# Kernel optimization log

Measured on AMD Instinct MI355X. Metric: run time of the kernel, lower is better.

The kernel has to match this reference:

```python
import jax, jax.numpy as jnp
import numpy as np
import math

NHEAD = 8
OUT = 64
EF = 64
IN = 256
NTYPES = 5
NH = 50000
NT = 100000
E = 800000
NEG_SLOPE = 0.2

def _uniform(key, shape, fan):
    # matches reset(): uniform(-stdv, stdv), stdv = sqrt(6/(fan_in+fan_out)) over last two dims
    stdv = math.sqrt(6.0 / (shape[-2] + shape[-1]))
    return jax.random.uniform(key, shape, jnp.float32, -stdv, stdv)

def setup_inputs() -> dict:
    key = jax.random.key(0)
    ks = jax.random.split(key, 12)
    head_feature = jax.random.normal(ks[0], (NH, IN), jnp.float32)
    tail_feature = jax.random.normal(ks[1], (NT, IN), jnp.float32)
    head_ind = jax.random.randint(ks[2], (E,), 0, NH)
    tail_ind = jax.random.randint(ks[3], (E,), 0, NT)
    tmp_edge = jax.random.randint(ks[4], (E,), 0, NTYPES)
    edge_emb = _uniform(ks[5], (NTYPES, EF), None)
    W = _uniform(ks[6], (IN, OUT * NHEAD), None)
    W_e = _uniform(ks[7], (EF, EF * NHEAD), None)
    a_l = _uniform(ks[8], (1, NHEAD, OUT), None)
    a_r = _uniform(ks[9], (1, NHEAD, OUT), None)
    a_e = _uniform(ks[10], (1, NHEAD, EF), None)
    return {"head_feature": head_feature, "tail_feature": tail_feature,
            "head_ind": head_ind, "tail_ind": tail_ind, "tmp_edge": tmp_edge,
            "edge_emb": edge_emb, "W": W, "W_e": W_e,
            "a_l": a_l, "a_r": a_r, "a_e": a_e}

def reference(head_feature, tail_feature, head_ind, tail_ind, tmp_edge,
              edge_emb, W, W_e, a_l, a_r, a_e):
    n_head_nodes = head_feature.shape[0]
    # projections (dropout is identity in eval)
    h_head = (head_feature @ W).reshape(-1, NHEAD, OUT)   # [NH, H, D]
    h_tail = (tail_feature @ W).reshape(-1, NHEAD, OUT)   # [NT, H, D]
    e = (edge_emb @ W_e).reshape(-1, NHEAD, EF)           # [T, H, EF]
    # per-edge attention logits, all heads at once: [E, H]
    h_l = jnp.sum(a_l * h_head, axis=-1)[head_ind]
    h_r = jnp.sum(a_r * h_tail, axis=-1)[tail_ind]
    h_e = jnp.sum(a_e * e, axis=-1)[tmp_edge]
    att = jax.nn.leaky_relu(h_l + h_r + h_e, NEG_SLOPE)
    # sparse (per-destination-row) softmax, vectorized over heads
    seg_max = jax.ops.segment_max(att, head_ind, num_segments=n_head_nodes)
    att = jnp.exp(att - seg_max[head_ind])
    denom = jax.ops.segment_sum(att, head_ind, num_segments=n_head_nodes)
    att = att / denom[head_ind]                           # [E, H]
    # weighted aggregation per head (small fixed loop over heads)
    outs = [jax.ops.segment_sum(att[:, n:n + 1] * h_tail[tail_ind, n, :],
                                head_ind, num_segments=n_head_nodes)
            for n in range(NHEAD)]
    out = jnp.stack(outs, axis=1).reshape(n_head_nodes, -1)  # [NH, H*D]
    return out, att
```

## Files before the change

### kernel.cpp

```cpp
#include <hip/hip_runtime.h>

#define NH 50000
#define NT 100000
#define NE 800000
#define MPAD 100096

typedef __attribute__((ext_vector_type(8))) short bf16x8;
typedef __attribute__((ext_vector_type(4))) float f32x4;
typedef __attribute__((ext_vector_type(8))) unsigned short u16x8;

__device__ __forceinline__ unsigned short f2bf(float f){
  unsigned int u = __float_as_uint(f);
  u += 0x7FFFu + ((u >> 16) & 1u);
  return (unsigned short)(u >> 16);
}

__device__ __forceinline__ void fma8(float* acc, float w, uint4 pk){
  acc[0] += w*__uint_as_float(pk.x<<16); acc[1] += w*__uint_as_float(pk.x&0xFFFF0000u);
  acc[2] += w*__uint_as_float(pk.y<<16); acc[3] += w*__uint_as_float(pk.y&0xFFFF0000u);
  acc[4] += w*__uint_as_float(pk.z<<16); acc[5] += w*__uint_as_float(pk.z&0xFFFF0000u);
  acc[6] += w*__uint_as_float(pk.w<<16); acc[7] += w*__uint_as_float(pk.w&0xFFFF0000u);
}

__device__ __forceinline__ void gl2lds16(const unsigned short* g, unsigned short* l){
  __builtin_amdgcn_global_load_lds(
      (const __attribute__((address_space(1))) void*)g,
      (__attribute__((address_space(3))) void*)l, 16, 0, 0);
}

__global__ void k_prep(const float* __restrict__ W, const float* __restrict__ W_e,
                       const float* __restrict__ edge_emb,
                       const float* __restrict__ a_l, const float* __restrict__ a_r,
                       const float* __restrict__ a_e,
                       unsigned short* __restrict__ wlr_t,
                       float* __restrict__ h_e){
  __shared__ float s_al[512], s_ar[512], s_ae[512], s_wef[512];
  int t = threadIdx.x;
  for (int i=t;i<512;i+=256){ s_al[i]=a_l[i]; s_ar[i]=a_r[i]; s_ae[i]=a_e[i]; }
  __syncthreads();
  { int k = t;
    for (int h=0;h<8;h++){
      float accl=0.f, accr=0.f;
      for (int d=0; d<64; d++){
        float w = W[k*512 + h*64 + d];
        accl += w*s_al[h*64+d];
        accr += w*s_ar[h*64+d];
      }
      wlr_t[h*256 + k]     = f2bf(accl);
      wlr_t[(8+h)*256 + k] = f2bf(accr);
    }
  }
  if (t<64){
    for (int h=0;h<8;h++){
      float acc=0.f;
      for (int f=0; f<64; f++) acc += W_e[t*512 + h*64 + f]*s_ae[h*64+f];
      s_wef[t*8+h]=acc;
    }
  }
  __syncthreads();
  if (t<40){
    int ty=t>>3, h=t&7;
    float acc=0.f;
    for (int k2=0;k2<64;k2++) acc += edge_emb[ty*64+k2]*s_wef[k2*8+h];
    h_e[t]=acc;
  }
}

__global__ void k_wt(const float* __restrict__ W, unsigned short* __restrict__ Wt){
  int n = blockIdx.x, k = threadIdx.x;
  Wt[n*256+k] = f2bf(W[k*512+n]);
}

__global__ __launch_bounds__(256) void k_cvt(const float* __restrict__ A,
                                             unsigned short* __restrict__ Ab){
  size_t g = (size_t)blockIdx.x*256 + threadIdx.x;
  const float* src = A + g*8;
  float4 v0 = *(const float4*)(src);
  float4 v1 = *(const float4*)(src + 4);
  u16x8 s;
  s[0]=f2bf(v0.x); s[1]=f2bf(v0.y); s[2]=f2bf(v0.z); s[3]=f2bf(v0.w);
  s[4]=f2bf(v1.x); s[5]=f2bf(v1.y); s[6]=f2bf(v1.z); s[7]=f2bf(v1.w);
  *(u16x8*)(Ab + g*8) = s;
}

__global__ __launch_bounds__(256) void k_hl(const float* __restrict__ head_f,
      const unsigned short* __restrict__ wlr_t, float* __restrict__ h_l){
  __shared__ unsigned short As[256*64];
  __shared__ unsigned short Bs[16*256];
  int t = threadIdx.x;
  int wave = t>>6, lane = t&63;
  int lr = lane&15, lq = lane>>4;
  long r0 = (long)blockIdx.x*256;

#pragma unroll
  for (int i=0;i<2;i++){
    int q = i*256 + t;
    int c = q>>5, un = q&31;
    float4 v = *(const float4*)(wlr_t + c*256 + un*8);
    int u = un ^ (c&7);
    *(float4*)((char*)Bs + c*512 + u*16) = v;
  }

  f32x4 acc[4];
#pragma unroll
  for (int mf=0;mf<4;mf++) acc[mf]=(f32x4){0.f,0.f,0.f,0.f};

  for (int kt=0; kt<4; kt++){
    __syncthreads();
#pragma unroll
    for (int i=0;i<16;i++){
      int q = i*256+t;
      int row = q>>4, cg = q&15;
      long gr = r0 + row;
      float4 v = make_float4(0.f,0.f,0.f,0.f);
      if (gr < NH) v = *(const float4*)(head_f + gr*256 + kt*64 + cg*4);
      int u = (cg>>1) ^ (row&7);
      ushort4 sv;
      sv.x=f2bf(v.x); sv.y=f2bf(v.y); sv.z=f2bf(v.z); sv.w=f2bf(v.w);
      *(ushort4*)((char*)As + row*128 + u*16 + (cg&1)*8) = sv;
    }
    __syncthreads();
#pragma unroll
    for (int ks=0;ks<2;ks++){
      int un = kt*8 + ks*4 + lq;
      int cu = un ^ (lr&7);
      bf16x8 bfr = *(const bf16x8*)((const char*)Bs + lr*512 + cu*16);
#pragma unroll
      for (int mf=0;mf<4;mf++){
        int r = wave*64 + mf*16 + lr;
        int u = (ks*4+lq) ^ (r&7);
        bf16x8 afr = *(const bf16x8*)((const char*)As + r*128 + u*16);
        acc[mf] = __builtin_amdgcn_mfma_f32_16x16x32_bf16(afr, bfr, acc[mf], 0,0,0);
      }
    }
  }
#pragma unroll
  for (int mf=0;mf<4;mf++)
#pragma unroll
    for (int j=0;j<4;j++){
      long grow = r0 + wave*64 + mf*16 + lq*4 + j;
      if (grow < NH && lr < 8) h_l[grow*8+lr] = acc[mf][j];
    }
}

__global__ __launch_bounds__(256) void k_gemm3(const unsigned short* __restrict__ A_bf,
      const unsigned short* __restrict__ Wt, const float* __restrict__ a_r_g,
      unsigned short* __restrict__ Cout, float* __restrict__ h_r){
  __shared__ unsigned short As[2][128*64];
  int t = threadIdx.x;
  int wave = t>>6, lane = t&63;
  int lr = lane & 15, lq = lane >> 4;

  int bid = blockIdx.x;
  int wg  = (bid & 7)*391 + (bid >> 3);
  int m0 = (wg >> 2)*128;
  int n0 = (wg & 3)*128;
  int wm = (wave>>1)*64, wn = (wave&1)*64;

  f32x4 acc[4][4];
#pragma unroll
  for (int mf=0;mf<4;mf++)
#pragma unroll
    for (int nf=0;nf<4;nf++) acc[mf][nf] = (f32x4){0.f,0.f,0.f,0.f};

  bf16x8 bcur[8], bnxt[8];

#define STAGEA(buf, kt) do { \
    _Pragma("unroll") \
    for (int i=0;i<4;i++){ \
      int v = wave*256 + i*64 + lane; \
      int row = v>>3, un = (v&7) ^ (row&7); \
      gl2lds16(A_bf + (size_t)(m0+row)*256 + (kt)*64 + un*8, \
               &As[buf][(wave*256 + i*64)*8]); \
    } } while(0)

#define LOADB(kt, dst) do { \
    _Pragma("unroll") \
    for (int ks=0;ks<2;ks++) \
      _Pragma("unroll") \
      for (int nf=0;nf<4;nf++){ \
        int c = wn + nf*16 + lr; \
        (dst)[ks*4+nf] = *(const bf16x8*)(Wt + (size_t)(n0+c)*256 + ((kt)*8+ks*4+lq)*8); \
      } } while(0)

  STAGEA(0, 0);
  LOADB(0, bcur);
  __syncthreads();
  int cur = 0;
  for (int kt=0; kt<4; kt++){
    if (kt < 3){ STAGEA(cur^1, kt+1); LOADB(kt+1, bnxt); }
#pragma unroll
    for (int ks=0;ks<2;ks++){
      bf16x8 af[4];
#pragma unroll
      for (int mf=0;mf<4;mf++){
        int r = wm + mf*16 + lr;
        int u = (ks*4 + lq) ^ (r&7);
        af[mf] = *(const bf16x8*)((const char*)As[cur] + r*128 + u*16);
      }
#pragma unroll
      for (int mf=0;mf<4;mf++)
#pragma unroll
        for (int nf=0;nf<4;nf++)
          acc[mf][nf] = __builtin_amdgcn_mfma_f32_16x16x32_bf16(af[mf], bcur[ks*4+nf], acc[mf][nf], 0,0,0);
    }
    __syncthreads();
    if (kt < 3){
      cur ^= 1;
#pragma unroll
      for (int i=0;i<8;i++) bcur[i] = bnxt[i];
    }
  }
#undef STAGEA
#undef LOADB

  {
    int h = (n0 + wn) >> 6;
    float w[4];
#pragma unroll
    for (int nf=0;nf<4;nf++) w[nf] = a_r_g[h*64 + nf*16 + lr];
#pragma unroll
    for (int mf=0;mf<4;mf++)
#pragma unroll
      for (int j=0;j<4;j++){
        float s = acc[mf][0][j]*w[0] + acc[mf][1][j]*w[1]
                + acc[mf][2][j]*w[2] + acc[mf][3][j]*w[3];
        s += __shfl_xor(s, 1); s += __shfl_xor(s, 2);
        s += __shfl_xor(s, 4); s += __shfl_xor(s, 8);
        int gr = m0 + wm + mf*16 + lq*4 + j;
        if (lr == 0 && gr < NT) h_r[(size_t)gr*8 + h] = s;
      }
  }

  unsigned short* Cs = &As[0][0];
#pragma unroll
  for (int mf=0;mf<4;mf++)
#pragma unroll
    for (int nf=0;nf<4;nf++)
#pragma unroll
      for (int j=0;j<4;j++){
        int row = wm + mf*16 + lq*4 + j;
        int cb  = (wn + nf*16 + lr)*2;
        *(unsigned short*)((char*)Cs + row*256 + (cb ^ ((row&12)<<3))) = f2bf(acc[mf][nf][j]);
      }
  __syncthreads();
#pragma unroll
  for (int i=0;i<8;i++){
    int v = i*256 + t;
    int row = v>>4, u = v&15;
    uint4 val = *(const uint4*)((const char*)Cs + row*256 + ((u*16) ^ ((row&12)<<3)));
    *(uint4*)(Cout + (size_t)(m0+row)*512 + n0 + u*8) = val;
  }
}

__global__ void k_hist(const int* __restrict__ head_ind, int* __restrict__ cnt){
  int e = blockIdx.x*256 + threadIdx.x;
  atomicAdd(&cnt[head_ind[e]], 1);
}

__global__ void k_scan1(const int* __restrict__ cnt, int* __restrict__ bsum){
  __shared__ int s[256];
  int b=blockIdx.x, t=threadIdx.x, g=b*256+t;
  s[t] = (g<NH)? cnt[g] : 0;
  __syncthreads();
  for (int off=128; off>0; off>>=1){ if (t<off) s[t]+=s[t+off]; __syncthreads(); }
  if (t==0) bsum[b]=s[0];
}
__global__ void k_scan2(int* __restrict__ bsum, int nb){
  __shared__ int s[256];
  int t=threadIdx.x;
  int v = (t<nb)? bsum[t] : 0;
  s[t]=v; __syncthreads();
  for (int off=1; off<256; off<<=1){
    int u = (t>=off)? s[t-off] : 0; __syncthreads();
    s[t]+=u; __syncthreads();
  }
  if (t<nb) bsum[t] = s[t]-v;
}
__global__ void k_scan3(const int* __restrict__ cnt, const int* __restrict__ bsum,
                        int* __restrict__ offs, int* __restrict__ cur){
  __shared__ int s[256];
  int b=blockIdx.x, t=threadIdx.x, g=b*256+t;
  int v=(g<NH)? cnt[g] : 0;
  s[t]=v; __syncthreads();
  for (int off=1; off<256; off<<=1){
    int u=(t>=off)? s[t-off] : 0; __syncthreads();
    s[t]+=u; __syncthreads();
  }
  int excl = s[t]-v + bsum[b];
  if (g<NH){
    offs[g]=excl; cur[g]=excl;
    if (g==NH-1) offs[NH]=excl+v;
  }
}

__global__ void k_logit2(const int* __restrict__ head_ind, const int* __restrict__ tail_ind,
                         const int* __restrict__ tmp_edge,
                         const float* __restrict__ h_l, const float* __restrict__ h_r,
                         const float* __restrict__ h_e,
                         int* __restrict__ cur,
                         float* __restrict__ att_csr,
                         int* __restrict__ edge_of, int* __restrict__ tail_s){
  int g = blockIdx.x*256 + threadIdx.x;
  int e = g>>3, h = g&7, l = threadIdx.x&63;
  int hd = head_ind[e], tl = tail_ind[e], ty = tmp_edge[e];
  float v = h_l[hd*8+h] + h_r[(size_t)tl*8+h] + h_e[ty*8+h];
  v = v > 0.f ? v : 0.2f*v;
  int p = 0;
  if (h==0) p = atomicAdd(&cur[hd], 1);
  p = __shfl(p, l & ~7);
  att_csr[p*8+h] = v;
  if (h==0){ edge_of[p]=e; tail_s[p]=tl; }
}

__global__ __launch_bounds__(256) void k_agg3(const int* __restrict__ offs,
      const int* __restrict__ edge_of, const int* __restrict__ tail_s,
      const float* __restrict__ att_csr,
      const unsigned short* __restrict__ h_tail,
      float* __restrict__ att, float* __restrict__ out){
  int t = threadIdx.x;
  int l = t & 63;
  int i = blockIdx.x*4 + (t>>6);
  int h = l & 7, hq = l >> 3;
  int s0 = offs[i];
  int deg = offs[i+1] - s0;

  float m = -1e30f;
  for (int q = hq; q < deg; q += 8) m = fmaxf(m, att_csr[(s0+q)*8 + h]);
  m = fmaxf(m, __shfl_xor(m, 8));
  m = fmaxf(m, __shfl_xor(m, 16));
  m = fmaxf(m, __shfl_xor(m, 32));
  float sum = 0.f;
  for (int q = hq; q < deg; q += 8) sum += __expf(att_csr[(s0+q)*8 + h] - m);
  sum += __shfl_xor(sum, 8); sum += __shfl_xor(sum, 16); sum += __shfl_xor(sum, 32);
  float r = (deg > 0) ? 1.f/sum : 0.f;

  float mh = __shfl(m, hq), rh = __shfl(r, hq);
  bool wlane = (l & 7) == 0;
  float acc[8];
#pragma unroll
  for (int c=0;c<8;c++) acc[c]=0.f;

  int j = 0;
  for (; j+8 <= deg; j += 8){
    int   tt[8]; float aa[8]; uint4 rr[8];
#pragma unroll
    for (int q2=0;q2<8;q2++){ int p=s0+j+q2; tt[q2]=tail_s[p]; aa[q2]=att_csr[p*8+hq]; }
#pragma unroll
    for (int q2=0;q2<8;q2++) rr[q2] = *(const uint4*)(h_tail + (size_t)tt[q2]*512 + l*8);
#pragma unroll
    for (int q2=0;q2<8;q2++){
      float w = __expf(aa[q2]-mh)*rh;
      if (wlane) __builtin_nontemporal_store(w, &att[(size_t)edge_of[s0+j+q2]*8 + hq]);
      fma8(acc, w, rr[q2]);
    }
  }
  for (; j+2 <= deg; j += 2){
    int p0=s0+j, p1=p0+1;
    int t0=tail_s[p0], t1=tail_s[p1];
    float a0=att_csr[p0*8+hq], a1=att_csr[p1*8+hq];
    uint4 r0 = *(const uint4*)(h_tail + (size_t)t0*512 + l*8);
    uint4 r1 = *(const uint4*)(h_tail + (size_t)t1*512 + l*8);
    float w0=__expf(a0-mh)*rh, w1=__expf(a1-mh)*rh;
    if (wlane){
      __builtin_nontemporal_store(w0, &att[(size_t)edge_of[p0]*8 + hq]);
      __builtin_nontemporal_store(w1, &att[(size_t)edge_of[p1]*8 + hq]);
    }
    fma8(acc, w0, r0);
    fma8(acc, w1, r1);
  }
  if (j < deg){
    int p0 = s0+j;
    int t0 = tail_s[p0];
    float a0 = att_csr[p0*8 + hq];
    uint4 r0 = *(const uint4*)(h_tail + (size_t)t0*512 + l*8);
    float w0 = __expf(a0 - mh) * rh;
    if (wlane) __builtin_nontemporal_store(w0, &att[(size_t)edge_of[p0]*8 + hq]);
    fma8(acc, w0, r0);
  }
  float* o = out + (size_t)i*512 + l*8;
  f32x4 v0 = {acc[0],acc[1],acc[2],acc[3]};
  f32x4 v1 = {acc[4],acc[5],acc[6],acc[7]};
  __builtin_nontemporal_store(v0, (f32x4*)o);
  __builtin_nontemporal_store(v1, (f32x4*)(o+4));
}

extern "C" void kernel_launch(void* const* d_in, const int* in_sizes, int n_in,
                              void* d_out, int out_size, void* d_ws, size_t ws_size,
                              hipStream_t stream) {
  const float* head_f   = (const float*)d_in[0];
  const float* tail_f   = (const float*)d_in[1];
  const int*   head_ind = (const int*)d_in[2];
  const int*   tail_ind = (const int*)d_in[3];
  const int*   tmp_edge = (const int*)d_in[4];
  const float* edge_emb = (const float*)d_in[5];
  const float* W        = (const float*)d_in[6];
  const float* W_e      = (const float*)d_in[7];
  const float* a_l      = (const float*)d_in[8];
  const float* a_r      = (const float*)d_in[9];
  const float* a_e      = (const float*)d_in[10];

  float* out = (float*)d_out;
  float* att = out + (size_t)NH*512;
  unsigned short* A_bf = (unsigned short*)d_out;

  char* ws = (char*)d_ws;
  auto alloc = [&](size_t bytes)->char*{ char* p = ws; ws += (bytes+511)&~(size_t)511; return p; };
  unsigned short* Wt    = (unsigned short*)alloc((size_t)512*256*2);
  unsigned short* wlr_t = (unsigned short*)alloc((size_t)16*256*2);
  float* h_e            = (float*)alloc(512);
  float* h_l            = (float*)alloc((size_t)NH*8*4);
  float* h_r            = (float*)alloc((size_t)NT*8*4);
  unsigned short* h_tail= (unsigned short*)alloc((size_t)MPAD*512*2);
  int* cnt              = (int*)alloc((size_t)NH*4);
  int* offs             = (int*)alloc((size_t)(NH+1)*4);
  int* cur              = (int*)alloc((size_t)NH*4);
  int* bsum             = (int*)alloc(1024);
  int* edge_of          = (int*)alloc((size_t)NE*4);
  int* tail_s           = (int*)alloc((size_t)NE*4);
  float* att_csr        = (float*)alloc((size_t)NE*8*4);

  hipMemsetAsync(cnt, 0, (size_t)NH*4, stream);
  k_prep<<<1,256,0,stream>>>(W, W_e, edge_emb, a_l, a_r, a_e, wlr_t, h_e);
  k_wt<<<512,256,0,stream>>>(W, Wt);
  k_cvt<<<12500,256,0,stream>>>(tail_f, A_bf);
  k_hl<<<(NH+255)/256,256,0,stream>>>(head_f, wlr_t, h_l);
  k_gemm3<<<3128,256,0,stream>>>(A_bf, Wt, a_r, h_tail, h_r);
  k_hist<<<NE/256,256,0,stream>>>(head_ind, cnt);
  k_scan1<<<196,256,0,stream>>>(cnt, bsum);
  k_scan2<<<1,256,0,stream>>>(bsum, 196);
  k_scan3<<<196,256,0,stream>>>(cnt, bsum, offs, cur);
  k_logit2<<<NE*8/256,256,0,stream>>>(head_ind, tail_ind, tmp_edge, h_l, h_r, h_e,
                                      cur, att_csr, edge_of, tail_s);
  k_agg3<<<NH/4,256,0,stream>>>(offs, edge_of, tail_s, att_csr, h_tail, att, out);
}
```

Baseline: 438.5 us.

## Split aggregation into two half-head passes and stage full-K A tile in GEMM

The aggregation kernel is split into two launches, each gathering half of every h_tail row (heads 0-3, then 4-7), so each pass touches a smaller gathered working set that may stay in cache. The first pass also writes the normalized attention and saves per-row max and reciprocal sums for the second pass. The GEMM now loads the whole 128x256 A tile into LDS once instead of double-buffering K slices, with B fragments loaded per k-step and an occupancy hint. The split costs an extra launch, a second walk over the CSR index arrays, and more LDS per block.

```diff
diff --git a/kernel.cpp b/kernel.cpp
--- a/kernel.cpp
+++ b/kernel.cpp
@@ -8,6 +8,7 @@
 typedef __attribute__((ext_vector_type(8))) short bf16x8;
 typedef __attribute__((ext_vector_type(4))) float f32x4;
 typedef __attribute__((ext_vector_type(8))) unsigned short u16x8;
+typedef __attribute__((ext_vector_type(4))) unsigned int u32x4;
 
 __device__ __forceinline__ unsigned short f2bf(float f){
   unsigned int u = __float_as_uint(f);
@@ -15,11 +16,9 @@
   return (unsigned short)(u >> 16);
 }
 
-__device__ __forceinline__ void fma8(float* acc, float w, uint4 pk){
+__device__ __forceinline__ void fma4(float* acc, float w, uint2 pk){
   acc[0] += w*__uint_as_float(pk.x<<16); acc[1] += w*__uint_as_float(pk.x&0xFFFF0000u);
   acc[2] += w*__uint_as_float(pk.y<<16); acc[3] += w*__uint_as_float(pk.y&0xFFFF0000u);
-  acc[4] += w*__uint_as_float(pk.z<<16); acc[5] += w*__uint_as_float(pk.z&0xFFFF0000u);
-  acc[6] += w*__uint_as_float(pk.w<<16); acc[7] += w*__uint_as_float(pk.w&0xFFFF0000u);
 }
 
 __device__ __forceinline__ void gl2lds16(const unsigned short* g, unsigned short* l){
@@ -143,10 +142,10 @@
     }
 }
 
-__global__ __launch_bounds__(256) void k_gemm3(const unsigned short* __restrict__ A_bf,
+__global__ __launch_bounds__(256,2) void k_gemm4(const unsigned short* __restrict__ A_bf,
       const unsigned short* __restrict__ Wt, const float* __restrict__ a_r_g,
       unsigned short* __restrict__ Cout, float* __restrict__ h_r){
-  __shared__ unsigned short As[2][128*64];
+  __shared__ unsigned short As[128*256];
   int t = threadIdx.x;
   int wave = t>>6, lane = t&63;
   int lr = lane & 15, lq = lane >> 4;
@@ -157,62 +156,40 @@
   int n0 = (wg & 3)*128;
   int wm = (wave>>1)*64, wn = (wave&1)*64;
 
+#pragma unroll
+  for (int i=0;i<16;i++){
+    int v = i*256 + t;
+    int row = v>>5, un = (v&31) ^ (row&7);
+    gl2lds16(A_bf + (size_t)(m0+row)*256 + un*8, &As[(size_t)(i*256 + wave*64)*8]);
+  }
+
   f32x4 acc[4][4];
 #pragma unroll
   for (int mf=0;mf<4;mf++)
 #pragma unroll
     for (int nf=0;nf<4;nf++) acc[mf][nf] = (f32x4){0.f,0.f,0.f,0.f};
 
-  bf16x8 bcur[8], bnxt[8];
-
-#define STAGEA(buf, kt) do { \
-    _Pragma("unroll") \
-    for (int i=0;i<4;i++){ \
-      int v = wave*256 + i*64 + lane; \
-      int row = v>>3, un = (v&7) ^ (row&7); \
-      gl2lds16(A_bf + (size_t)(m0+row)*256 + (kt)*64 + un*8, \
-               &As[buf][(wave*256 + i*64)*8]); \
-    } } while(0)
-
-#define LOADB(kt, dst) do { \
-    _Pragma("unroll") \
-    for (int ks=0;ks<2;ks++) \
-      _Pragma("unroll") \
-      for (int nf=0;nf<4;nf++){ \
-        int c = wn + nf*16 + lr; \
-        (dst)[ks*4+nf] = *(const bf16x8*)(Wt + (size_t)(n0+c)*256 + ((kt)*8+ks*4+lq)*8); \
-      } } while(0)
-
-  STAGEA(0, 0);
-  LOADB(0, bcur);
-  __syncthreads();
-  int cur = 0;
-  for (int kt=0; kt<4; kt++){
-    if (kt < 3){ STAGEA(cur^1, kt+1); LOADB(kt+1, bnxt); }
-#pragma unroll
-    for (int ks=0;ks<2;ks++){
-      bf16x8 af[4];
-#pragma unroll
-      for (int mf=0;mf<4;mf++){
-        int r = wm + mf*16 + lr;
-        int u = (ks*4 + lq) ^ (r&7);
-        af[mf] = *(const bf16x8*)((const char*)As[cur] + r*128 + u*16);
-      }
-#pragma unroll
-      for (int mf=0;mf<4;mf++)
-#pragma unroll
-        for (int nf=0;nf<4;nf++)
-          acc[mf][nf] = __builtin_amdgcn_mfma_f32_16x16x32_bf16(af[mf], bcur[ks*4+nf], acc[mf][nf], 0,0,0);
-    }
-    __syncthreads();
-    if (kt < 3){
-      cur ^= 1;
-#pragma unroll
-      for (int i=0;i<8;i++) bcur[i] = bnxt[i];
-    }
-  }
-#undef STAGEA
-#undef LOADB
+  __syncthreads();
+
+#pragma unroll
+  for (int ks=0; ks<8; ks++){
+    bf16x8 bfr[4];
+#pragma unroll
+    for (int nf=0;nf<4;nf++)
+      bfr[nf] = *(const bf16x8*)(Wt + (size_t)(n0 + wn + nf*16 + lr)*256 + ks*32 + lq*8);
+    bf16x8 af[4];
+#pragma unroll
+    for (int mf=0;mf<4;mf++){
+      int r = wm + mf*16 + lr;
+      int un = (ks*4 + lq) ^ (r&7);
+      af[mf] = *(const bf16x8*)(As + (size_t)(r*32 + un)*8);
+    }
+#pragma unroll
+    for (int mf=0;mf<4;mf++)
+#pragma unroll
+      for (int nf=0;nf<4;nf++)
+        acc[mf][nf] = __builtin_amdgcn_mfma_f32_16x16x32_bf16(af[mf], bfr[nf], acc[mf][nf], 0,0,0);
+  }
 
   {
     int h = (n0 + wn) >> 6;
@@ -232,7 +209,8 @@
       }
   }
 
-  unsigned short* Cs = &As[0][0];
+  __syncthreads();
+  unsigned short* Cs = As;
 #pragma unroll
   for (int mf=0;mf<4;mf++)
 #pragma unroll
@@ -248,8 +226,8 @@
   for (int i=0;i<8;i++){
     int v = i*256 + t;
     int row = v>>4, u = v&15;
-    uint4 val = *(const uint4*)((const char*)Cs + row*256 + ((u*16) ^ ((row&12)<<3)));
-    *(uint4*)(Cout + (size_t)(m0+row)*512 + n0 + u*8) = val;
+    u32x4 val = *(const u32x4*)((const char*)Cs + row*256 + ((u*16) ^ ((row&12)<<3)));
+    *(u32x4*)(Cout + (size_t)(m0+row)*512 + n0 + u*8) = val;
   }
 }
 
@@ -313,76 +291,112 @@
   if (h==0){ edge_of[p]=e; tail_s[p]=tl; }
 }
 
-__global__ __launch_bounds__(256) void k_agg3(const int* __restrict__ offs,
+__global__ __launch_bounds__(256) void k_aggA(const int* __restrict__ offs,
       const int* __restrict__ edge_of, const int* __restrict__ tail_s,
       const float* __restrict__ att_csr,
       const unsigned short* __restrict__ h_tail,
+      float* __restrict__ mr,
       float* __restrict__ att, float* __restrict__ out){
   int t = threadIdx.x;
   int l = t & 63;
   int i = blockIdx.x*4 + (t>>6);
-  int h = l & 7, hq = l >> 3;
+  int h = l & 7, sq = l >> 3;
   int s0 = offs[i];
   int deg = offs[i+1] - s0;
 
   float m = -1e30f;
-  for (int q = hq; q < deg; q += 8) m = fmaxf(m, att_csr[(s0+q)*8 + h]);
+  for (int q = sq; q < deg; q += 8) m = fmaxf(m, att_csr[(s0+q)*8 + h]);
   m = fmaxf(m, __shfl_xor(m, 8));
   m = fmaxf(m, __shfl_xor(m, 16));
   m = fmaxf(m, __shfl_xor(m, 32));
   float sum = 0.f;
-  for (int q = hq; q < deg; q += 8) sum += __expf(att_csr[(s0+q)*8 + h] - m);
+  for (int q = sq; q < deg; q += 8) sum += __expf(att_csr[(s0+q)*8 + h] - m);
   sum += __shfl_xor(sum, 8); sum += __shfl_xor(sum, 16); sum += __shfl_xor(sum, 32);
   float r = (deg > 0) ? 1.f/sum : 0.f;
-
-  float mh = __shfl(m, hq), rh = __shfl(r, hq);
-  bool wlane = (l & 7) == 0;
-  float acc[8];
-#pragma unroll
-  for (int c=0;c<8;c++) acc[c]=0.f;
+  if (l < 8){ mr[(size_t)i*16 + l*2] = m; mr[(size_t)i*16 + l*2 + 1] = r; }
+
+  for (int q = sq; q < deg; q += 8){
+    int p = s0 + q;
+    float a = __expf(att_csr[p*8 + h] - m) * r;
+    __builtin_nontemporal_store(a, &att[(size_t)edge_of[p]*8 + h]);
+  }
+
+  int hw = l >> 4;
+  float mh = __shfl(m, hw), rh = __shfl(r, hw);
+  float acc[4];
+#pragma unroll
+  for (int c=0;c<4;c++) acc[c]=0.f;
 
   int j = 0;
-  for (; j+8 <= deg; j += 8){
-    int   tt[8]; float aa[8]; uint4 rr[8];
-#pragma unroll
-    for (int q2=0;q2<8;q2++){ int p=s0+j+q2; tt[q2]=tail_s[p]; aa[q2]=att_csr[p*8+hq]; }
-#pragma unroll
-    for (int q2=0;q2<8;q2++) rr[q2] = *(const uint4*)(h_tail + (size_t)tt[q2]*512 + l*8);
-#pragma unroll
-    for (int q2=0;q2<8;q2++){
-      float w = __expf(aa[q2]-mh)*rh;
-      if (wlane) __builtin_nontemporal_store(w, &att[(size_t)edge_of[s0+j+q2]*8 + hq]);
-      fma8(acc, w, rr[q2]);
-    }
-  }
-  for (; j+2 <= deg; j += 2){
-    int p0=s0+j, p1=p0+1;
-    int t0=tail_s[p0], t1=tail_s[p1];
-    float a0=att_csr[p0*8+hq], a1=att_csr[p1*8+hq];
-    uint4 r0 = *(const uint4*)(h_tail + (size_t)t0*512 + l*8);
-    uint4 r1 = *(const uint4*)(h_tail + (size_t)t1*512 + l*8);
-    float w0=__expf(a0-mh)*rh, w1=__expf(a1-mh)*rh;
-    if (wlane){
-      __builtin_nontemporal_store(w0, &att[(size_t)edge_of[p0]*8 + hq]);
-      __builtin_nontemporal_store(w1, &att[(size_t)edge_of[p1]*8 + hq]);
-    }
-    fma8(acc, w0, r0);
-    fma8(acc, w1, r1);
-  }
-  if (j < deg){
+  for (; j+4 <= deg; j += 4){
+    int p0=s0+j, p1=p0+1, p2=p0+2, p3=p0+3;
+    int t0=tail_s[p0], t1=tail_s[p1], t2=tail_s[p2], t3=tail_s[p3];
+    float a0=att_csr[p0*8+hw], a1=att_csr[p1*8+hw];
+    float a2=att_csr[p2*8+hw], a3=att_csr[p3*8+hw];
+    uint2 r0 = *(const uint2*)(h_tail + (size_t)t0*512 + l*4);
+    uint2 r1 = *(const uint2*)(h_tail + (size_t)t1*512 + l*4);
+    uint2 r2 = *(const uint2*)(h_tail + (size_t)t2*512 + l*4);
+    uint2 r3 = *(const uint2*)(h_tail + (size_t)t3*512 + l*4);
+    fma4(acc, __expf(a0-mh)*rh, r0);
+    fma4(acc, __expf(a1-mh)*rh, r1);
+    fma4(acc, __expf(a2-mh)*rh, r2);
+    fma4(acc, __expf(a3-mh)*rh, r3);
+  }
+  for (; j < deg; j++){
     int p0 = s0+j;
     int t0 = tail_s[p0];
-    float a0 = att_csr[p0*8 + hq];
-    uint4 r0 = *(const uint4*)(h_tail + (size_t)t0*512 + l*8);
-    float w0 = __expf(a0 - mh) * rh;
-    if (wlane) __builtin_nontemporal_store(w0, &att[(size_t)edge_of[p0]*8 + hq]);
-    fma8(acc, w0, r0);
-  }
-  float* o = out + (size_t)i*512 + l*8;
+    float a0 = att_csr[p0*8 + hw];
+    uint2 r0 = *(const uint2*)(h_tail + (size_t)t0*512 + l*4);
+    fma4(acc, __expf(a0 - mh)*rh, r0);
+  }
   f32x4 v0 = {acc[0],acc[1],acc[2],acc[3]};
-  f32x4 v1 = {acc[4],acc[5],acc[6],acc[7]};
-  __builtin_nontemporal_store(v0, (f32x4*)o);
-  __builtin_nontemporal_store(v1, (f32x4*)(o+4));
+  __builtin_nontemporal_store(v0, (f32x4*)(out + (size_t)i*512 + l*4));
+}
+
+__global__ __launch_bounds__(256) void k_aggB(const int* __restrict__ offs,
+      const int* __restrict__ tail_s,
+      const float* __restrict__ att_csr,
+      const unsigned short* __restrict__ h_tail,
+      const float* __restrict__ mr,
+      float* __restrict__ out){
+  int t = threadIdx.x;
+  int l = t & 63;
+  int i = blockIdx.x*4 + (t>>6);
+  int hw = 4 + (l >> 4);
+  int s0 = offs[i];
+  int deg = offs[i+1] - s0;
+
+  float2 st = *(const float2*)(mr + (size_t)i*16 + hw*2);
+  float mh = st.x, rh = st.y;
+
+  float acc[4];
+#pragma unroll
+  for (int c=0;c<4;c++) acc[c]=0.f;
+
+  int j = 0;
+  for (; j+4 <= deg; j += 4){
+    int p0=s0+j, p1=p0+1, p2=p0+2, p3=p0+3;
+    int t0=tail_s[p0], t1=tail_s[p1], t2=tail_s[p2], t3=tail_s[p3];
+    float a0=att_csr[p0*8+hw], a1=att_csr[p1*8+hw];
+    float a2=att_csr[p2*8+hw], a3=att_csr[p3*8+hw];
+    uint2 r0 = *(const uint2*)(h_tail + (size_t)t0*512 + 256 + l*4);
+    uint2 r1 = *(const uint2*)(h_tail + (size_t)t1*512 + 256 + l*4);
+    uint2 r2 = *(const uint2*)(h_tail + (size_t)t2*512 + 256 + l*4);
+    uint2 r3 = *(const uint2*)(h_tail + (size_t)t3*512 + 256 + l*4);
+    fma4(acc, __expf(a0-mh)*rh, r0);
+    fma4(acc, __expf(a1-mh)*rh, r1);
+    fma4(acc, __expf(a2-mh)*rh, r2);
+    fma4(acc, __expf(a3-mh)*rh, r3);
+  }
+  for (; j < deg; j++){
+    int p0 = s0+j;
+    int t0 = tail_s[p0];
+    float a0 = att_csr[p0*8 + hw];
+    uint2 r0 = *(const uint2*)(h_tail + (size_t)t0*512 + 256 + l*4);
+    fma4(acc, __expf(a0 - mh)*rh, r0);
+  }
+  f32x4 v0 = {acc[0],acc[1],acc[2],acc[3]};
+  __builtin_nontemporal_store(v0, (f32x4*)(out + (size_t)i*512 + 256 + l*4));
 }
 
 extern "C" void kernel_launch(void* const* d_in, const int* in_sizes, int n_in,
@@ -419,18 +433,20 @@
   int* edge_of          = (int*)alloc((size_t)NE*4);
   int* tail_s           = (int*)alloc((size_t)NE*4);
   float* att_csr        = (float*)alloc((size_t)NE*8*4);
+  float* mr             = (float*)alloc((size_t)NH*16*4);
 
   hipMemsetAsync(cnt, 0, (size_t)NH*4, stream);
   k_prep<<<1,256,0,stream>>>(W, W_e, edge_emb, a_l, a_r, a_e, wlr_t, h_e);
   k_wt<<<512,256,0,stream>>>(W, Wt);
   k_cvt<<<12500,256,0,stream>>>(tail_f, A_bf);
   k_hl<<<(NH+255)/256,256,0,stream>>>(head_f, wlr_t, h_l);
-  k_gemm3<<<3128,256,0,stream>>>(A_bf, Wt, a_r, h_tail, h_r);
+  k_gemm4<<<3128,256,0,stream>>>(A_bf, Wt, a_r, h_tail, h_r);
   k_hist<<<NE/256,256,0,stream>>>(head_ind, cnt);
   k_scan1<<<196,256,0,stream>>>(cnt, bsum);
   k_scan2<<<1,256,0,stream>>>(bsum, 196);
   k_scan3<<<196,256,0,stream>>>(cnt, bsum, offs, cur);
   k_logit2<<<NE*8/256,256,0,stream>>>(head_ind, tail_ind, tmp_edge, h_l, h_r, h_e,
                                       cur, att_csr, edge_of, tail_s);
-  k_agg3<<<NH/4,256,0,stream>>>(offs, edge_of, tail_s, att_csr, h_tail, att, out);
-}
+  k_aggA<<<NH/4,256,0,stream>>>(offs, edge_of, tail_s, att_csr, h_tail, mr, att, out);
+  k_aggB<<<NH/4,256,0,stream>>>(offs, tail_s, att_csr, h_tail, mr, out);
+}
```

Result: slower. 463.3 us (+5.7%).

## Merge prep/convert/histogram and GEMM/h_l kernels into block-dispatched launches; retune aggregation loop

Applied to the files above, without the earlier changes.

Independent small kernels (bf16 conversion, degree histogram, weight transpose, attention-vector prep) become one launch that picks its role by block index. The tail-projection GEMM and the h_l GEMM become a second combined launch sharing one LDS buffer. This cuts launch overhead and lets the independent stages overlap. The aggregation kernel now unrolls its gather by 4 instead of 8 and reads CSR streams with nontemporal loads. This adds a hazard: wlr_t is written by the prep block inside the same launch that converts data, and is then read in the next launch, so stream ordering still holds.

```diff
diff --git a/kernel.cpp b/kernel.cpp
--- a/kernel.cpp
+++ b/kernel.cpp
@@ -8,6 +8,7 @@
 typedef __attribute__((ext_vector_type(8))) short bf16x8;
 typedef __attribute__((ext_vector_type(4))) float f32x4;
 typedef __attribute__((ext_vector_type(8))) unsigned short u16x8;
+typedef __attribute__((ext_vector_type(4))) unsigned int u32x4;
 
 __device__ __forceinline__ unsigned short f2bf(float f){
   unsigned int u = __float_as_uint(f);
@@ -28,69 +29,180 @@
       (__attribute__((address_space(3))) void*)l, 16, 0, 0);
 }
 
-__global__ void k_prep(const float* __restrict__ W, const float* __restrict__ W_e,
-                       const float* __restrict__ edge_emb,
-                       const float* __restrict__ a_l, const float* __restrict__ a_r,
-                       const float* __restrict__ a_e,
-                       unsigned short* __restrict__ wlr_t,
-                       float* __restrict__ h_e){
+__global__ __launch_bounds__(256) void k_fuse1(
+      const float* __restrict__ tail_f, unsigned short* __restrict__ A_bf,
+      const int* __restrict__ head_ind, int* __restrict__ cnt,
+      const float* __restrict__ W, unsigned short* __restrict__ Wt,
+      const float* __restrict__ W_e, const float* __restrict__ edge_emb,
+      const float* __restrict__ a_l, const float* __restrict__ a_r,
+      const float* __restrict__ a_e,
+      unsigned short* __restrict__ wlr_t, float* __restrict__ h_e){
   __shared__ float s_al[512], s_ar[512], s_ae[512], s_wef[512];
+  int b = blockIdx.x, t = threadIdx.x;
+  if (b < 12500){
+    size_t g = (size_t)b*256 + t;
+    const float* src = tail_f + g*8;
+    float4 v0 = *(const float4*)(src);
+    float4 v1 = *(const float4*)(src + 4);
+    u16x8 s;
+    s[0]=f2bf(v0.x); s[1]=f2bf(v0.y); s[2]=f2bf(v0.z); s[3]=f2bf(v0.w);
+    s[4]=f2bf(v1.x); s[5]=f2bf(v1.y); s[6]=f2bf(v1.z); s[7]=f2bf(v1.w);
+    *(u16x8*)(A_bf + g*8) = s;
+  } else if (b < 15625){
+    int e = (b-12500)*256 + t;
+    atomicAdd(&cnt[head_ind[e]], 1);
+  } else if (b < 16137){
+    int n = b - 15625, k = t;
+    Wt[n*256+k] = f2bf(W[k*512+n]);
+  } else {
+    for (int i=t;i<512;i+=256){ s_al[i]=a_l[i]; s_ar[i]=a_r[i]; s_ae[i]=a_e[i]; }
+    __syncthreads();
+    { int k = t;
+      for (int h=0;h<8;h++){
+        float accl=0.f, accr=0.f;
+        for (int d=0; d<64; d++){
+          float w = W[k*512 + h*64 + d];
+          accl += w*s_al[h*64+d];
+          accr += w*s_ar[h*64+d];
+        }
+        wlr_t[h*256 + k]     = f2bf(accl);
+        wlr_t[(8+h)*256 + k] = f2bf(accr);
+      }
+    }
+    if (t<64){
+      for (int h=0;h<8;h++){
+        float acc=0.f;
+        for (int f=0; f<64; f++) acc += W_e[t*512 + h*64 + f]*s_ae[h*64+f];
+        s_wef[t*8+h]=acc;
+      }
+    }
+    __syncthreads();
+    if (t<40){
+      int ty=t>>3, h=t&7;
+      float acc=0.f;
+      for (int k2=0;k2<64;k2++) acc += edge_emb[ty*64+k2]*s_wef[k2*8+h];
+      h_e[t]=acc;
+    }
+  }
+}
+
+__device__ __forceinline__ void gemm3_body(unsigned short* smem, int bid,
+      const unsigned short* __restrict__ A_bf, const unsigned short* __restrict__ Wt,
+      const float* __restrict__ a_r_g, unsigned short* __restrict__ Cout,
+      float* __restrict__ h_r){
+  unsigned short* Asb[2] = { smem, smem + 8192 };
   int t = threadIdx.x;
-  for (int i=t;i<512;i+=256){ s_al[i]=a_l[i]; s_ar[i]=a_r[i]; s_ae[i]=a_e[i]; }
+  int wave = t>>6, lane = t&63;
+  int lr = lane & 15, lq = lane >> 4;
+
+  int wg  = (bid & 7)*391 + (bid >> 3);
+  int m0 = (wg >> 2)*128;
+  int n0 = (wg & 3)*128;
+  int wm = (wave>>1)*64, wn = (wave&1)*64;
+
+  f32x4 acc[4][4];
+#pragma unroll
+  for (int mf=0;mf<4;mf++)
+#pragma unroll
+    for (int nf=0;nf<4;nf++) acc[mf][nf] = (f32x4){0.f,0.f,0.f,0.f};
+
+  bf16x8 bcur[8], bnxt[8];
+
+#define STAGEA(buf, kt) do { \
+    _Pragma("unroll") \
+    for (int i=0;i<4;i++){ \
+      int v = wave*256 + i*64 + lane; \
+      int row = v>>3, un = (v&7) ^ (row&7); \
+      gl2lds16(A_bf + (size_t)(m0+row)*256 + (kt)*64 + un*8, \
+               &Asb[buf][(wave*256 + i*64)*8]); \
+    } } while(0)
+
+#define LOADB(kt, dst) do { \
+    _Pragma("unroll") \
+    for (int ks=0;ks<2;ks++) \
+      _Pragma("unroll") \
+      for (int nf=0;nf<4;nf++){ \
+        int c = wn + nf*16 + lr; \
+        (dst)[ks*4+nf] = *(const bf16x8*)(Wt + (size_t)(n0+c)*256 + ((kt)*8+ks*4+lq)*8); \
+      } } while(0)
+
+  STAGEA(0, 0);
+  LOADB(0, bcur);
   __syncthreads();
-  { int k = t;
-    for (int h=0;h<8;h++){
-      float accl=0.f, accr=0.f;
-      for (int d=0; d<64; d++){
-        float w = W[k*512 + h*64 + d];
-        accl += w*s_al[h*64+d];
-        accr += w*s_ar[h*64+d];
-      }
-      wlr_t[h*256 + k]     = f2bf(accl);
-      wlr_t[(8+h)*256 + k] = f2bf(accr);
-    }
-  }
-  if (t<64){
-    for (int h=0;h<8;h++){
-      float acc=0.f;
-      for (int f=0; f<64; f++) acc += W_e[t*512 + h*64 + f]*s_ae[h*64+f];
-      s_wef[t*8+h]=acc;
-    }
-  }
+  int cur = 0;
+  for (int kt=0; kt<4; kt++){
+    if (kt < 3){ STAGEA(cur^1, kt+1); LOADB(kt+1, bnxt); }
+#pragma unroll
+    for (int ks=0;ks<2;ks++){
+      bf16x8 af[4];
+#pragma unroll
+      for (int mf=0;mf<4;mf++){
+        int r = wm + mf*16 + lr;
+        int u = (ks*4 + lq) ^ (r&7);
+        af[mf] = *(const bf16x8*)((const char*)Asb[cur] + r*128 + u*16);
+      }
+#pragma unroll
+      for (int mf=0;mf<4;mf++)
+#pragma unroll
+        for (int nf=0;nf<4;nf++)
+          acc[mf][nf] = __builtin_amdgcn_mfma_f32_16x16x32_bf16(af[mf], bcur[ks*4+nf], acc[mf][nf], 0,0,0);
+    }
+    __syncthreads();
+    if (kt < 3){
+      cur ^= 1;
+#pragma unroll
+      for (int i=0;i<8;i++) bcur[i] = bnxt[i];
+    }
+  }
+#undef STAGEA
+#undef LOADB
+
+  {
+    int h = (n0 + wn) >> 6;
+    float w[4];
+#pragma unroll
+    for (int nf=0;nf<4;nf++) w[nf] = a_r_g[h*64 + nf*16 + lr];
+#pragma unroll
+    for (int mf=0;mf<4;mf++)
+#pragma unroll
+      for (int j=0;j<4;j++){
+        float s = acc[mf][0][j]*w[0] + acc[mf][1][j]*w[1]
+                + acc[mf][2][j]*w[2] + acc[mf][3][j]*w[3];
+        s += __shfl_xor(s, 1); s += __shfl_xor(s, 2);
+        s += __shfl_xor(s, 4); s += __shfl_xor(s, 8);
+        int gr = m0 + wm + mf*16 + lq*4 + j;
+        if (lr == 0 && gr < NT) h_r[(size_t)gr*8 + h] = s;
+      }
+  }
+
+  unsigned short* Cs = smem;
+#pragma unroll
+  for (int mf=0;mf<4;mf++)
+#pragma unroll
+    for (int nf=0;nf<4;nf++)
+#pragma unroll
+      for (int j=0;j<4;j++){
+        int row = wm + mf*16 + lq*4 + j;
+        int cb  = (wn + nf*16 + lr)*2;
+        *(unsigned short*)((char*)Cs + row*256 + (cb ^ ((row&12)<<3))) = f2bf(acc[mf][nf][j]);
+      }
   __syncthreads();
-  if (t<40){
-    int ty=t>>3, h=t&7;
-    float acc=0.f;
-    for (int k2=0;k2<64;k2++) acc += edge_emb[ty*64+k2]*s_wef[k2*8+h];
-    h_e[t]=acc;
-  }
-}
-
-__global__ void k_wt(const float* __restrict__ W, unsigned short* __restrict__ Wt){
-  int n = blockIdx.x, k = threadIdx.x;
-  Wt[n*256+k] = f2bf(W[k*512+n]);
-}
-
-__global__ __launch_bounds__(256) void k_cvt(const float* __restrict__ A,
-                                             unsigned short* __restrict__ Ab){
-  size_t g = (size_t)blockIdx.x*256 + threadIdx.x;
-  const float* src = A + g*8;
-  float4 v0 = *(const float4*)(src);
-  float4 v1 = *(const float4*)(src + 4);
-  u16x8 s;
-  s[0]=f2bf(v0.x); s[1]=f2bf(v0.y); s[2]=f2bf(v0.z); s[3]=f2bf(v0.w);
-  s[4]=f2bf(v1.x); s[5]=f2bf(v1.y); s[6]=f2bf(v1.z); s[7]=f2bf(v1.w);
-  *(u16x8*)(Ab + g*8) = s;
-}
-
-__global__ __launch_bounds__(256) void k_hl(const float* __restrict__ head_f,
-      const unsigned short* __restrict__ wlr_t, float* __restrict__ h_l){
-  __shared__ unsigned short As[256*64];
-  __shared__ unsigned short Bs[16*256];
+#pragma unroll
+  for (int i=0;i<8;i++){
+    int v = i*256 + t;
+    int row = v>>4, u = v&15;
+    u32x4 val = *(const u32x4*)((const char*)Cs + row*256 + ((u*16) ^ ((row&12)<<3)));
+    *(u32x4*)(Cout + (size_t)(m0+row)*512 + n0 + u*8) = val;
+  }
+}
+
+__device__ __forceinline__ void hl_body(unsigned short* As, unsigned short* Bs, int bid,
+      const float* __restrict__ head_f, const unsigned short* __restrict__ wlr_t,
+      float* __restrict__ h_l){
   int t = threadIdx.x;
   int wave = t>>6, lane = t&63;
   int lr = lane&15, lq = lane>>4;
-  long r0 = (long)blockIdx.x*256;
+  long r0 = (long)bid*256;
 
 #pragma unroll
   for (int i=0;i<2;i++){
@@ -143,119 +255,17 @@
     }
 }
 
-__global__ __launch_bounds__(256) void k_gemm3(const unsigned short* __restrict__ A_bf,
-      const unsigned short* __restrict__ Wt, const float* __restrict__ a_r_g,
-      unsigned short* __restrict__ Cout, float* __restrict__ h_r){
-  __shared__ unsigned short As[2][128*64];
-  int t = threadIdx.x;
-  int wave = t>>6, lane = t&63;
-  int lr = lane & 15, lq = lane >> 4;
-
-  int bid = blockIdx.x;
-  int wg  = (bid & 7)*391 + (bid >> 3);
-  int m0 = (wg >> 2)*128;
-  int n0 = (wg & 3)*128;
-  int wm = (wave>>1)*64, wn = (wave&1)*64;
-
-  f32x4 acc[4][4];
-#pragma unroll
-  for (int mf=0;mf<4;mf++)
-#pragma unroll
-    for (int nf=0;nf<4;nf++) acc[mf][nf] = (f32x4){0.f,0.f,0.f,0.f};
-
-  bf16x8 bcur[8], bnxt[8];
-
-#define STAGEA(buf, kt) do { \
-    _Pragma("unroll") \
-    for (int i=0;i<4;i++){ \
-      int v = wave*256 + i*64 + lane; \
-      int row = v>>3, un = (v&7) ^ (row&7); \
-      gl2lds16(A_bf + (size_t)(m0+row)*256 + (kt)*64 + un*8, \
-               &As[buf][(wave*256 + i*64)*8]); \
-    } } while(0)
-
-#define LOADB(kt, dst) do { \
-    _Pragma("unroll") \
-    for (int ks=0;ks<2;ks++) \
-      _Pragma("unroll") \
-      for (int nf=0;nf<4;nf++){ \
-        int c = wn + nf*16 + lr; \
-        (dst)[ks*4+nf] = *(const bf16x8*)(Wt + (size_t)(n0+c)*256 + ((kt)*8+ks*4+lq)*8); \
-      } } while(0)
-
-  STAGEA(0, 0);
-  LOADB(0, bcur);
-  __syncthreads();
-  int cur = 0;
-  for (int kt=0; kt<4; kt++){
-    if (kt < 3){ STAGEA(cur^1, kt+1); LOADB(kt+1, bnxt); }
-#pragma unroll
-    for (int ks=0;ks<2;ks++){
-      bf16x8 af[4];
-#pragma unroll
-      for (int mf=0;mf<4;mf++){
-        int r = wm + mf*16 + lr;
-        int u = (ks*4 + lq) ^ (r&7);
-        af[mf] = *(const bf16x8*)((const char*)As[cur] + r*128 + u*16);
-      }
-#pragma unroll
-      for (int mf=0;mf<4;mf++)
-#pragma unroll
-        for (int nf=0;nf<4;nf++)
-          acc[mf][nf] = __builtin_amdgcn_mfma_f32_16x16x32_bf16(af[mf], bcur[ks*4+nf], acc[mf][nf], 0,0,0);
-    }
-    __syncthreads();
-    if (kt < 3){
-      cur ^= 1;
-#pragma unroll
-      for (int i=0;i<8;i++) bcur[i] = bnxt[i];
-    }
-  }
-#undef STAGEA
-#undef LOADB
-
-  {
-    int h = (n0 + wn) >> 6;
-    float w[4];
-#pragma unroll
-    for (int nf=0;nf<4;nf++) w[nf] = a_r_g[h*64 + nf*16 + lr];
-#pragma unroll
-    for (int mf=0;mf<4;mf++)
-#pragma unroll
-      for (int j=0;j<4;j++){
-        float s = acc[mf][0][j]*w[0] + acc[mf][1][j]*w[1]
-                + acc[mf][2][j]*w[2] + acc[mf][3][j]*w[3];
-        s += __shfl_xor(s, 1); s += __shfl_xor(s, 2);
-        s += __shfl_xor(s, 4); s += __shfl_xor(s, 8);
-        int gr = m0 + wm + mf*16 + lq*4 + j;
-        if (lr == 0 && gr < NT) h_r[(size_t)gr*8 + h] = s;
-      }
-  }
-
-  unsigned short* Cs = &As[0][0];
-#pragma unroll
-  for (int mf=0;mf<4;mf++)
-#pragma unroll
-    for (int nf=0;nf<4;nf++)
-#pragma unroll
-      for (int j=0;j<4;j++){
-        int row = wm + mf*16 + lq*4 + j;
-        int cb  = (wn + nf*16 + lr)*2;
-        *(unsigned short*)((char*)Cs + row*256 + (cb ^ ((row&12)<<3))) = f2bf(acc[mf][nf][j]);
-      }
-  __syncthreads();
-#pragma unroll
-  for (int i=0;i<8;i++){
-    int v = i*256 + t;
-    int row = v>>4, u = v&15;
-    uint4 val = *(const uint4*)((const char*)Cs + row*256 + ((u*16) ^ ((row&12)<<3)));
-    *(uint4*)(Cout + (size_t)(m0+row)*512 + n0 + u*8) = val;
-  }
-}
-
-__global__ void k_hist(const int* __restrict__ head_ind, int* __restrict__ cnt){
-  int e = blockIdx.x*256 + threadIdx.x;
-  atomicAdd(&cnt[head_ind[e]], 1);
+__global__ __launch_bounds__(256) void k_fuse2(
+      const unsigned short* __restrict__ A_bf, const unsigned short* __restrict__ Wt,
+      const float* __restrict__ a_r_g, unsigned short* __restrict__ Cout,
+      float* __restrict__ h_r,
+      const float* __restrict__ head_f, const unsigned short* __restrict__ wlr_t,
+      float* __restrict__ h_l){
+  __shared__ __align__(16) unsigned short smem[20480];
+  if (blockIdx.x < 3128)
+    gemm3_body(smem, blockIdx.x, A_bf, Wt, a_r_g, Cout, h_r);
+  else
+    hl_body(smem, smem + 16384, blockIdx.x - 3128, head_f, wlr_t, h_l);
 }
 
 __global__ void k_scan1(const int* __restrict__ cnt, int* __restrict__ bsum){
@@ -326,12 +336,12 @@
   int deg = offs[i+1] - s0;
 
   float m = -1e30f;
-  for (int q = hq; q < deg; q += 8) m = fmaxf(m, att_csr[(s0+q)*8 + h]);
+  for (int q = hq; q < deg; q += 8) m = fmaxf(m, __builtin_nontemporal_load(&att_csr[(s0+q)*8 + h]));
   m = fmaxf(m, __shfl_xor(m, 8));
   m = fmaxf(m, __shfl_xor(m, 16));
   m = fmaxf(m, __shfl_xor(m, 32));
   float sum = 0.f;
-  for (int q = hq; q < deg; q += 8) sum += __expf(att_csr[(s0+q)*8 + h] - m);
+  for (int q = hq; q < deg; q += 8) sum += __expf(__builtin_nontemporal_load(&att_csr[(s0+q)*8 + h]) - m);
   sum += __shfl_xor(sum, 8); sum += __shfl_xor(sum, 16); sum += __shfl_xor(sum, 32);
   float r = (deg > 0) ? 1.f/sum : 0.f;
 
@@ -340,42 +350,37 @@
   float acc[8];
 #pragma unroll
   for (int c=0;c<8;c++) acc[c]=0.f;
-
   int j = 0;
-  for (; j+8 <= deg; j += 8){
-    int   tt[8]; float aa[8]; uint4 rr[8];
-#pragma unroll
-    for (int q2=0;q2<8;q2++){ int p=s0+j+q2; tt[q2]=tail_s[p]; aa[q2]=att_csr[p*8+hq]; }
-#pragma unroll
-    for (int q2=0;q2<8;q2++) rr[q2] = *(const uint4*)(h_tail + (size_t)tt[q2]*512 + l*8);
-#pragma unroll
-    for (int q2=0;q2<8;q2++){
-      float w = __expf(aa[q2]-mh)*rh;
-      if (wlane) __builtin_nontemporal_store(w, &att[(size_t)edge_of[s0+j+q2]*8 + hq]);
-      fma8(acc, w, rr[q2]);
-    }
-  }
-  for (; j+2 <= deg; j += 2){
-    int p0=s0+j, p1=p0+1;
-    int t0=tail_s[p0], t1=tail_s[p1];
-    float a0=att_csr[p0*8+hq], a1=att_csr[p1*8+hq];
+  for (; j+4 <= deg; j += 4){
+    int p0=s0+j, p1=p0+1, p2=p0+2, p3=p0+3;
+    int t0=__builtin_nontemporal_load(&tail_s[p0]), t1=__builtin_nontemporal_load(&tail_s[p1]);
+    int t2=__builtin_nontemporal_load(&tail_s[p2]), t3=__builtin_nontemporal_load(&tail_s[p3]);
+    float a0=__builtin_nontemporal_load(&att_csr[p0*8+hq]), a1=__builtin_nontemporal_load(&att_csr[p1*8+hq]);
+    float a2=__builtin_nontemporal_load(&att_csr[p2*8+hq]), a3=__builtin_nontemporal_load(&att_csr[p3*8+hq]);
     uint4 r0 = *(const uint4*)(h_tail + (size_t)t0*512 + l*8);
     uint4 r1 = *(const uint4*)(h_tail + (size_t)t1*512 + l*8);
+    uint4 r2 = *(const uint4*)(h_tail + (size_t)t2*512 + l*8);
+    uint4 r3 = *(const uint4*)(h_tail + (size_t)t3*512 + l*8);
     float w0=__expf(a0-mh)*rh, w1=__expf(a1-mh)*rh;
+    float w2=__expf(a2-mh)*rh, w3=__expf(a3-mh)*rh;
     if (wlane){
-      __builtin_nontemporal_store(w0, &att[(size_t)edge_of[p0]*8 + hq]);
-      __builtin_nontemporal_store(w1, &att[(size_t)edge_of[p1]*8 + hq]);
+      __builtin_nontemporal_store(w0, &att[(size_t)__builtin_nontemporal_load(&edge_of[p0])*8 + hq]);
+      __builtin_nontemporal_store(w1, &att[(size_t)__builtin_nontemporal_load(&edge_of[p1])*8 + hq]);
+      __builtin_nontemporal_store(w2, &att[(size_t)__builtin_nontemporal_load(&edge_of[p2])*8 + hq]);
+      __builtin_nontemporal_store(w3, &att[(size_t)__builtin_nontemporal_load(&edge_of[p3])*8 + hq]);
     }
     fma8(acc, w0, r0);
     fma8(acc, w1, r1);
-  }
-  if (j < deg){
+    fma8(acc, w2, r2);
+    fma8(acc, w3, r3);
+  }
+  for (; j < deg; j++){
     int p0 = s0+j;
-    int t0 = tail_s[p0];
-    float a0 = att_csr[p0*8 + hq];
+    int t0 = __builtin_nontemporal_load(&tail_s[p0]);
+    float a0 = __builtin_nontemporal_load(&att_csr[p0*8 + hq]);
     uint4 r0 = *(const uint4*)(h_tail + (size_t)t0*512 + l*8);
     float w0 = __expf(a0 - mh) * rh;
-    if (wlane) __builtin_nontemporal_store(w0, &att[(size_t)edge_of[p0]*8 + hq]);
+    if (wlane) __builtin_nontemporal_store(w0, &att[(size_t)__builtin_nontemporal_load(&edge_of[p0])*8 + hq]);
     fma8(acc, w0, r0);
   }
   float* o = out + (size_t)i*512 + l*8;
@@ -421,12 +426,9 @@
   float* att_csr        = (float*)alloc((size_t)NE*8*4);
 
   hipMemsetAsync(cnt, 0, (size_t)NH*4, stream);
-  k_prep<<<1,256,0,stream>>>(W, W_e, edge_emb, a_l, a_r, a_e, wlr_t, h_e);
-  k_wt<<<512,256,0,stream>>>(W, Wt);
-  k_cvt<<<12500,256,0,stream>>>(tail_f, A_bf);
-  k_hl<<<(NH+255)/256,256,0,stream>>>(head_f, wlr_t, h_l);
-  k_gemm3<<<3128,256,0,stream>>>(A_bf, Wt, a_r, h_tail, h_r);
-  k_hist<<<NE/256,256,0,stream>>>(head_ind, cnt);
+  k_fuse1<<<16138,256,0,stream>>>(tail_f, A_bf, head_ind, cnt, W, Wt,
+                                  W_e, edge_emb, a_l, a_r, a_e, wlr_t, h_e);
+  k_fuse2<<<3128+196,256,0,stream>>>(A_bf, Wt, a_r, h_tail, h_r, head_f, wlr_t, h_l);
   k_scan1<<<196,256,0,stream>>>(cnt, bsum);
   k_scan2<<<1,256,0,stream>>>(bsum, 196);
   k_scan3<<<196,256,0,stream>>>(cnt, bsum, offs, cur);
```

Measured after the change: 421.3 us. 3.9% less time.
